# Optimization experiments

Measured on AMD Instinct MI355X. Metric: run time of the kernel, lower is better.

The kernel has to match this reference:

```python
import jax, jax.numpy as jnp
import numpy as np

B, C, H, W = 8, 128, 64, 64


def setup_inputs() -> dict:
    key = jax.random.key(0)
    ks = jax.random.split(key, 8)
    s = 1.0 / np.sqrt(C)
    return {
        "x1": jax.random.normal(ks[0], (B, C, H, W), dtype=jnp.float32),
        "x2": jax.random.normal(ks[1], (B, C, H, W), dtype=jnp.float32),
        "Wq": jax.random.normal(ks[2], (C, C), dtype=jnp.float32) * s,
        "bq": jax.random.normal(ks[3], (C,), dtype=jnp.float32) * s,
        "Wk": jax.random.normal(ks[4], (C, C), dtype=jnp.float32) * s,
        "bk": jax.random.normal(ks[5], (C,), dtype=jnp.float32) * s,
        "Wv": jax.random.normal(ks[6], (C, C), dtype=jnp.float32) * s,
        "bv": jax.random.normal(ks[7], (C,), dtype=jnp.float32) * s,
    }


def reference(x1, x2, Wq, bq, Wk, bk, Wv, bv):
    b, c, h, w = x1.shape
    n = h * w
    # 1x1 conv == channel matmul per pixel; flatten spatial dims -> [b, c, n]
    x1f = x1.reshape(b, c, n)
    x2f = x2.reshape(b, c, n)
    q = jnp.einsum("oc,bcn->bno", Wq, x1f) + bq[None, None, :]  # [b, n, c]
    k = jnp.einsum("oc,bcn->bon", Wk, x2f) + bk[None, :, None]  # [b, c, n]
    v = jnp.einsum("oc,bcn->bon", Wv, x2f) + bv[None, :, None]  # [b, c, n]
    energy = jnp.einsum("bnc,bcm->bnm", q, k)                   # [b, n, n] (unscaled)
    attention = jax.nn.softmax(energy, axis=-1)
    # out[b,c,i] = sum_j v[b,c,j] * attention[b,i,j]
    out = jnp.einsum("bcj,bij->bci", v, attention)
    return out.reshape(b, c, h, w)
```

## Files before the change

kernel.cpp:

```cpp
#include <hip/hip_runtime.h>

typedef float f4 __attribute__((ext_vector_type(4)));
typedef float f16v __attribute__((ext_vector_type(16)));
typedef _Float16 hf;
typedef __fp16 fp16x2 __attribute__((ext_vector_type(2)));
typedef hf h8 __attribute__((ext_vector_type(8)));
typedef unsigned short ushort_t;
typedef unsigned int uint_t;
typedef uint_t u4 __attribute__((ext_vector_type(4)));

#define BATCH 8
#define CH 128
#define NPIX 4096
#define LOG2E 1.4426950408889634f
#define RESCALE_THR 8.0f

__device__ inline f16v mfma32h(h8 a, h8 b, f16v c) {
    return __builtin_amdgcn_mfma_f32_32x32x16_f16(a, b, c, 0, 0, 0);
}

__device__ inline uint_t pk2h(float a, float b) {
    fp16x2 pp = __builtin_amdgcn_cvt_pkrtz(a, b);
    union { fp16x2 v; uint_t u; } cv;
    cv.v = pp;
    return cv.u;
}

__device__ inline void pl32swap(uint_t& a, uint_t& b) {
    asm("v_permlane32_swap_b32 %0, %1" : "+v"(a), "+v"(b));
}

typedef __attribute__((address_space(3))) uint_t lds_uint;
typedef __attribute__((address_space(1))) const uint_t global_uint;
__device__ inline void dma16(const void* g, void* l) {
    __builtin_amdgcn_global_load_lds((global_uint*)g, (lds_uint*)l, 16, 0, 0);
}

__device__ inline ushort_t h2u(hf x) {
    union { hf h; ushort_t u; } cv;
    cv.h = x;
    return cv.u;
}

__global__ __launch_bounds__(256) void qkv_kernel(const float* __restrict__ x1,
                                                  const float* __restrict__ x2,
                                                  const float* __restrict__ Wq,
                                                  const float* __restrict__ Wk,
                                                  const float* __restrict__ Wv,
                                                  const float* __restrict__ bq,
                                                  const float* __restrict__ bk,
                                                  const float* __restrict__ bv,
                                                  hf* __restrict__ Qf, hf* __restrict__ Kf,
                                                  hf* __restrict__ Vf) {
    __shared__ __align__(16) ushort_t XH[64 * 128];
    __shared__ __align__(16) ushort_t XL[64 * 128];

    int bid = blockIdx.x;
    int m = bid >> 9;
    int rem = bid & 511;
    int b = rem & 7;
    int n0 = (rem >> 3) << 6;

    const float* X = ((m == 0) ? x1 : x2) + (size_t)b * CH * NPIX;
    const float* bias = (m == 0) ? bq : (m == 1) ? bk : bv;

    int tid = threadIdx.x;
#pragma unroll
    for (int r = 0; r < 8; ++r) {
        int c = 16 * r + (tid >> 4);
        int n4 = (tid & 15) << 2;
        f4 v = *(const f4*)&X[(size_t)c * NPIX + n0 + n4];
        int cs = c >> 3, cj = c & 7;
#pragma unroll
        for (int j = 0; j < 4; ++j) {
            int n = n4 + j;
            hf hi = (hf)v[j];
            hf lo = (hf)(v[j] - (float)hi);
            int ofs = n * 128 + ((cs ^ (n & 15)) << 3) + cj;
            XH[ofs] = h2u(hi);
            XL[ofs] = h2u(lo);
        }
    }

    int lane = tid & 63;
    int w = tid >> 6;
    int h = lane >> 5;
    int m32 = lane & 31;
    int o0 = w * 32;

    const float* Wsrc = (m == 0) ? Wq : (m == 1) ? Wk : Wv;
    float wscale = (m == 0) ? LOG2E : 1.0f;
    h8 wf[8];
    {
        const float* wrow = Wsrc + (size_t)(o0 + m32) * CH;
#pragma unroll
        for (int kc = 0; kc < 8; ++kc) {
            f4 a = *(const f4*)&wrow[kc * 16 + h * 8];
            f4 b2 = *(const f4*)&wrow[kc * 16 + h * 8 + 4];
            h8 t;
#pragma unroll
            for (int j = 0; j < 4; ++j) {
                t[j] = (hf)(a[j] * wscale);
                t[4 + j] = (hf)(b2[j] * wscale);
            }
            wf[kc] = t;
        }
    }

    __syncthreads();

    f16v acc[2];
#pragma unroll
    for (int g = 0; g < 2; ++g)
#pragma unroll
        for (int r = 0; r < 16; ++r) acc[g][r] = 0.f;

    int swzn = m32 & 15;
#pragma unroll
    for (int g = 0; g < 2; ++g) {
        int nrow = (g * 32 + m32) * 128;
#pragma unroll
        for (int kc = 0; kc < 8; ++kc) {
            int sofs = nrow + (((kc * 2 + h) ^ swzn) << 3);
            h8 xh = *(const h8*)&XH[sofs];
            h8 xl = *(const h8*)&XL[sofs];
            if (m == 2) {
                acc[g] = mfma32h(wf[kc], xh, acc[g]);
                acc[g] = mfma32h(wf[kc], xl, acc[g]);
            } else {
                acc[g] = mfma32h(xh, wf[kc], acc[g]);
                acc[g] = mfma32h(xl, wf[kc], acc[g]);
            }
        }
    }

    if (m < 2) {
        float bval = bias[o0 + m32] * ((m == 0) ? LOG2E : 1.0f);
        hf* Y = ((m == 0) ? Qf : Kf) + (size_t)b * NPIX * CH;
#pragma unroll
        for (int g = 0; g < 2; ++g)
#pragma unroll
            for (int r = 0; r < 16; ++r) {
                int n = n0 + g * 32 + (r & 3) + 8 * (r >> 2) + 4 * h;
                Y[(size_t)n * CH + o0 + m32] = (hf)(acc[g][r] + bval);
            }
    } else {
        hf* Yv = Vf + (size_t)b * CH * NPIX;
#pragma unroll
        for (int g = 0; g < 2; ++g)
#pragma unroll
            for (int r = 0; r < 16; ++r) {
                int o = o0 + (r & 3) + 8 * (r >> 2) + 4 * h;
                Yv[(size_t)o * NPIX + n0 + g * 32 + m32] = (hf)(acc[g][r] + bias[o]);
            }
    }
}

__global__ __launch_bounds__(256, 3) void attn_kernel(const hf* __restrict__ Qf,
                                                      const hf* __restrict__ Kf,
                                                      const hf* __restrict__ Vf,
                                                      hf* __restrict__ Opart,
                                                      float* __restrict__ Mpart,
                                                      float* __restrict__ Lpart) {
    __shared__ __align__(16) ushort_t smem[24576];

    int tid = threadIdx.x;
    int lane = tid & 63;
    int w = tid >> 6;
    int h = lane >> 5;
    int m32 = lane & 31;

    int idx = blockIdx.x;
    int b = idx & 7;
    int ks = (idx >> 3) & 3;
    int qt = idx >> 5;
    int q0 = (qt << 7) + w * 32;
    int k0g = ks << 10;

    const hf* Qb = Qf + (size_t)b * NPIX * CH;
    const hf* Kb = Kf + (size_t)b * NPIX * CH;
    const hf* Vb = Vf + (size_t)b * CH * NPIX;

    h8 qf[8];
#pragma unroll
    for (int kc = 0; kc < 8; ++kc)
        qf[kc] = *(const h8*)&Qb[(size_t)(q0 + m32) * CH + kc * 16 + h * 8];

    const hf* pK[2];
    const hf* pV[2];
#pragma unroll
    for (int a = 0; a < 2; ++a) {
        int chunk_hi = w * 2 + a;
        int rowk = chunk_hi * 4 + (lane >> 4);
        int lck = (lane & 15) ^ (rowk & 15);
        pK[a] = Kb + (size_t)(k0g + rowk) * CH + lck * 8;
        int rowv = chunk_hi * 16 + (lane >> 2);
        int lcv = (lane & 3) ^ (rowv & 3) ^ ((rowv >> 2) & 1);
        pV[a] = Vb + (size_t)rowv * NPIX + k0g + lcv * 8;
    }

#pragma unroll
    for (int tp = 0; tp < 2; ++tp) {
#pragma unroll
        for (int a = 0; a < 2; ++a) {
            dma16(pK[a], &smem[tp * 4096 + (w * 2 + a) * 512]);
            dma16(pV[a], &smem[12288 + tp * 4096 + (w * 2 + a) * 512]);
            pK[a] += 32 * CH;
            pV[a] += 32;
        }
    }

    f16v accO[4];
#pragma unroll
    for (int ct = 0; ct < 4; ++ct)
#pragma unroll
        for (int r = 0; r < 16; ++r) accO[ct][r] = 0.f;
    float mprev = -1e30f;
    float lsum = 0.f;

    int pvs[2];
#pragma unroll
    for (int g2 = 0; g2 < 2; ++g2)
        pvs[g2] = (g2 * 2 + h) ^ (m32 & 3) ^ ((m32 >> 2) & 1);

    int br = 0, bw = 2;
    for (int t = 0; t < 32; ++t) {
        if (t < 31) asm volatile("s_waitcnt vmcnt(4) lgkmcnt(0)" ::: "memory");
        else        asm volatile("s_waitcnt vmcnt(0) lgkmcnt(0)" ::: "memory");
        __builtin_amdgcn_s_barrier();
        __builtin_amdgcn_sched_barrier(0);

        if (t < 30) {
#pragma unroll
            for (int a = 0; a < 2; ++a) {
                dma16(pK[a], &smem[bw * 4096 + (w * 2 + a) * 512]);
                dma16(pV[a], &smem[12288 + bw * 4096 + (w * 2 + a) * 512]);
                pK[a] += 32 * CH;
                pV[a] += 32;
            }
        }
        const ushort_t* kb = smem + br * 4096;
        const ushort_t* vb = smem + 12288 + br * 4096;

        f16v acc;
#pragma unroll
        for (int r = 0; r < 16; ++r) acc[r] = 0.f;
        __builtin_amdgcn_s_setprio(1);
#pragma unroll
        for (int kc = 0; kc < 8; ++kc) {
            int pA = (kc * 2 + h) ^ (m32 & 15);
            h8 ahi = *(const h8*)&kb[m32 * 128 + pA * 8];
            acc = mfma32h(ahi, qf[kc], acc);
        }
        __builtin_amdgcn_s_setprio(0);

        float ta = fmaxf(fmaxf(acc[0], acc[1]), acc[2]);
        float tb = fmaxf(fmaxf(acc[3], acc[4]), acc[5]);
        ta = fmaxf(fmaxf(ta, acc[6]), acc[7]);
        tb = fmaxf(fmaxf(tb, acc[8]), acc[9]);
        ta = fmaxf(fmaxf(ta, acc[10]), acc[11]);
        tb = fmaxf(fmaxf(tb, acc[12]), acc[13]);
        ta = fmaxf(fmaxf(ta, acc[14]), acc[15]);
        float tmax = fmaxf(ta, tb);
        if (__any(tmax > mprev + RESCALE_THR)) {
            float tx = fmaxf(tmax, __shfl_xor(tmax, 32));
            float mnew = fmaxf(mprev, tx);
            float alpha = exp2f(mprev - mnew);
            lsum *= alpha;
#pragma unroll
            for (int ct = 0; ct < 4; ++ct)
#pragma unroll
                for (int r = 0; r < 16; ++r) accO[ct][r] *= alpha;
            mprev = mnew;
        }

        uint_t pk[8];
        float ps0 = 0.f, ps1 = 0.f;
#pragma unroll
        for (int t2 = 0; t2 < 8; ++t2) {
            float e0 = exp2f(acc[2 * t2] - mprev);
            float e1 = exp2f(acc[2 * t2 + 1] - mprev);
            ps0 += e0;
            ps1 += e1;
            pk[t2] = pk2h(e0, e1);
        }
        lsum += ps0 + ps1;

        pl32swap(pk[0], pk[2]);
        pl32swap(pk[1], pk[3]);
        pl32swap(pk[4], pk[6]);
        pl32swap(pk[5], pk[7]);
        h8 pbp[2];
#pragma unroll
        for (int g2 = 0; g2 < 2; ++g2) {
            u4 fv;
            fv[0] = pk[g2 * 4 + 0];
            fv[1] = pk[g2 * 4 + 1];
            fv[2] = pk[g2 * 4 + 2];
            fv[3] = pk[g2 * 4 + 3];
            __builtin_memcpy(&pbp[g2], &fv, 16);
        }

        __builtin_amdgcn_s_setprio(1);
#pragma unroll
        for (int g2 = 0; g2 < 2; ++g2) {
            int pv = pvs[g2];
#pragma unroll
            for (int ct = 0; ct < 4; ++ct) {
                h8 av = *(const h8*)&vb[(ct * 32 + m32) * 32 + pv * 8];
                accO[ct] = mfma32h(av, pbp[g2], accO[ct]);
            }
        }
        __builtin_amdgcn_s_setprio(0);

        br = (br == 2) ? 0 : br + 1;
        bw = (bw == 2) ? 0 : bw + 1;
    }

    lsum += __shfl_xor(lsum, 32);

    size_t base = (((size_t)ks * 8 + b) * 32 + qt) * 16384;
    size_t mlb = (((size_t)ks * 8 + b) * 32 + qt) * 128;
    int q = w * 32 + m32;
#pragma unroll
    for (int ct = 0; ct < 4; ++ct)
#pragma unroll
        for (int r = 0; r < 16; ++r) {
            int ch = ct * 32 + (r & 3) + 8 * (r >> 2) + 4 * h;
            Opart[base + ch * 128 + q] = (hf)accO[ct][r];
        }
    if (h == 0) {
        Mpart[mlb + q] = mprev;
        Lpart[mlb + q] = lsum;
    }
}

__global__ __launch_bounds__(256) void combine_kernel(const hf* __restrict__ Opart,
                                                      const float* __restrict__ Mp,
                                                      const float* __restrict__ Lp,
                                                      float* __restrict__ out) {
    int idx = blockIdx.x;
    int chh = idx & 1;
    int b = (idx >> 1) & 7;
    int qt = idx >> 4;
    int tid = threadIdx.x;
    int q8 = (tid & 15) << 3;
    int chl = tid >> 4;

    size_t tile = (size_t)b * 32 + qt;

    float Marr[4][8], Larr[4][8];
#pragma unroll
    for (int p = 0; p < 4; ++p) {
        const float* mp_ = Mp + ((size_t)p * 256 + tile) * 128 + q8;
        const float* lp_ = Lp + ((size_t)p * 256 + tile) * 128 + q8;
        f4 ma = *(const f4*)mp_;
        f4 mb = *(const f4*)(mp_ + 4);
        f4 la = *(const f4*)lp_;
        f4 lb = *(const f4*)(lp_ + 4);
#pragma unroll
        for (int j = 0; j < 4; ++j) {
            Marr[p][j] = ma[j];
            Marr[p][4 + j] = mb[j];
            Larr[p][j] = la[j];
            Larr[p][4 + j] = lb[j];
        }
    }

    float wgt[4][8];
#pragma unroll
    for (int j = 0; j < 8; ++j) {
        float M = fmaxf(fmaxf(Marr[0][j], Marr[1][j]), fmaxf(Marr[2][j], Marr[3][j]));
        float L = 0.f;
#pragma unroll
        for (int p = 0; p < 4; ++p) {
            float w_ = exp2f(Marr[p][j] - M);
            wgt[p][j] = w_;
            L += w_ * Larr[p][j];
        }
        float rd = 1.0f / L;
#pragma unroll
        for (int p = 0; p < 4; ++p) wgt[p][j] *= rd;
    }

    const hf* ob[4];
#pragma unroll
    for (int p = 0; p < 4; ++p) ob[p] = Opart + ((size_t)p * 256 + tile) * 16384 + q8;
    float* O = out + (size_t)b * CH * NPIX + (size_t)qt * 128 + q8;

#pragma unroll
    for (int it = 0; it < 4; ++it) {
        int ch = chh * 64 + it * 16 + chl;
        union { u4 u; h8 v; } o4[4];
#pragma unroll
        for (int p = 0; p < 4; ++p) o4[p].u = *(const u4*)&ob[p][(size_t)ch * 128];
        f4 r0, r1;
#pragma unroll
        for (int j = 0; j < 8; ++j) {
            float s = 0.f;
#pragma unroll
            for (int p = 0; p < 4; ++p) s += wgt[p][j] * (float)o4[p].v[j];
            if (j < 4) r0[j] = s;
            else r1[j - 4] = s;
        }
        float* dst = O + (size_t)ch * NPIX;
        *(f4*)dst = r0;
        *(f4*)(dst + 4) = r1;
    }
}

extern "C" void kernel_launch(void* const* d_in, const int* in_sizes, int n_in,
                              void* d_out, int out_size, void* d_ws, size_t ws_size,
                              hipStream_t stream) {
    const float* x1 = (const float*)d_in[0];
    const float* x2 = (const float*)d_in[1];
    const float* Wq = (const float*)d_in[2];
    const float* bq = (const float*)d_in[3];
    const float* Wk = (const float*)d_in[4];
    const float* bk = (const float*)d_in[5];
    const float* Wv = (const float*)d_in[6];
    const float* bv = (const float*)d_in[7];
    float* outp = (float*)d_out;

    const size_t N = (size_t)BATCH * NPIX * CH;
    hf* Qf = (hf*)d_ws;
    hf* Kf = Qf + N;
    hf* Vf = Qf + 2 * N;
    hf* Opart = Qf + 3 * N;
    float* Mp = (float*)(Opart + (size_t)4 * 8 * 32 * 16384);
    float* Lp = Mp + (size_t)4 * 8 * 32 * 128;

    qkv_kernel<<<3 * BATCH * (NPIX / 64), 256, 0, stream>>>(x1, x2, Wq, Wk, Wv,
                                                            bq, bk, bv, Qf, Kf, Vf);
    attn_kernel<<<BATCH * 4 * (NPIX / 128), 256, 0, stream>>>(Qf, Kf, Vf, Opart, Mp, Lp);
    combine_kernel<<<2 * BATCH * (NPIX / 128), 256, 0, stream>>>(Opart, Mp, Lp, outp);
}
```

Measured before the change: 209.9 us.

## Halve key splits and deepen attention LDS pipeline to four buffers

The attention kernel now splits the key range into 2 parts instead of 4, so each block walks 2048 keys. The combine kernel merges 2 partials instead of 4, which cuts partial-output traffic. The K/V staging ring grows from 3 to 4 LDS buffers with an explicitly unrolled schedule that keeps three tiles in flight, and occupancy drops from 3 to 2 blocks per CU because LDS use rises. The grid halves to 512 blocks, which may underfill the GPU's CUs and leave more of the latency exposed.

```diff
diff --git a/kernel.cpp b/kernel.cpp
--- a/kernel.cpp
+++ b/kernel.cpp
@@ -41,6 +41,13 @@
     cv.h = x;
     return cv.u;
 }
+
+#define WAITB(vm)                                                          \
+    do {                                                                   \
+        asm volatile("s_waitcnt vmcnt(" #vm ") lgkmcnt(0)" ::: "memory");  \
+        __builtin_amdgcn_s_barrier();                                      \
+        __builtin_amdgcn_sched_barrier(0);                                 \
+    } while (0)
 
 __global__ __launch_bounds__(256) void qkv_kernel(const float* __restrict__ x1,
                                                   const float* __restrict__ x2,
@@ -156,13 +163,13 @@
     }
 }
 
-__global__ __launch_bounds__(256, 3) void attn_kernel(const hf* __restrict__ Qf,
+__global__ __launch_bounds__(256, 2) void attn_kernel(const hf* __restrict__ Qf,
                                                       const hf* __restrict__ Kf,
                                                       const hf* __restrict__ Vf,
                                                       hf* __restrict__ Opart,
                                                       float* __restrict__ Mpart,
                                                       float* __restrict__ Lpart) {
-    __shared__ __align__(16) ushort_t smem[24576];
+    __shared__ __align__(16) ushort_t smem[32768];
 
     int tid = threadIdx.x;
     int lane = tid & 63;
@@ -172,10 +179,10 @@
 
     int idx = blockIdx.x;
     int b = idx & 7;
-    int ks = (idx >> 3) & 3;
-    int qt = idx >> 5;
+    int ks = (idx >> 3) & 1;
+    int qt = idx >> 4;
     int q0 = (qt << 7) + w * 32;
-    int k0g = ks << 10;
+    int k0g = ks << 11;
 
     const hf* Qb = Qf + (size_t)b * NPIX * CH;
     const hf* Kb = Kf + (size_t)b * NPIX * CH;
@@ -199,17 +206,6 @@
         pV[a] = Vb + (size_t)rowv * NPIX + k0g + lcv * 8;
     }
 
-#pragma unroll
-    for (int tp = 0; tp < 2; ++tp) {
-#pragma unroll
-        for (int a = 0; a < 2; ++a) {
-            dma16(pK[a], &smem[tp * 4096 + (w * 2 + a) * 512]);
-            dma16(pV[a], &smem[12288 + tp * 4096 + (w * 2 + a) * 512]);
-            pK[a] += 32 * CH;
-            pV[a] += 32;
-        }
-    }
-
     f16v accO[4];
 #pragma unroll
     for (int ct = 0; ct < 4; ++ct)
@@ -223,24 +219,19 @@
     for (int g2 = 0; g2 < 2; ++g2)
         pvs[g2] = (g2 * 2 + h) ^ (m32 & 3) ^ ((m32 >> 2) & 1);
 
-    int br = 0, bw = 2;
-    for (int t = 0; t < 32; ++t) {
-        if (t < 31) asm volatile("s_waitcnt vmcnt(4) lgkmcnt(0)" ::: "memory");
-        else        asm volatile("s_waitcnt vmcnt(0) lgkmcnt(0)" ::: "memory");
-        __builtin_amdgcn_s_barrier();
-        __builtin_amdgcn_sched_barrier(0);
-
-        if (t < 30) {
-#pragma unroll
-            for (int a = 0; a < 2; ++a) {
-                dma16(pK[a], &smem[bw * 4096 + (w * 2 + a) * 512]);
-                dma16(pV[a], &smem[12288 + bw * 4096 + (w * 2 + a) * 512]);
-                pK[a] += 32 * CH;
-                pV[a] += 32;
-            }
-        }
-        const ushort_t* kb = smem + br * 4096;
-        const ushort_t* vb = smem + 12288 + br * 4096;
+    auto stage = [&](int bufw) {
+#pragma unroll
+        for (int a = 0; a < 2; ++a) {
+            dma16(pK[a], &smem[bufw * 4096 + (w * 2 + a) * 512]);
+            dma16(pV[a], &smem[16384 + bufw * 4096 + (w * 2 + a) * 512]);
+            pK[a] += 32 * CH;
+            pV[a] += 32;
+        }
+    };
+
+    auto comp = [&](int bufr) {
+        const ushort_t* kb = smem + bufr * 4096;
+        const ushort_t* vb = smem + 16384 + bufr * 4096;
 
         f16v acc;
 #pragma unroll
@@ -312,10 +303,22 @@
             }
         }
         __builtin_amdgcn_s_setprio(0);
-
-        br = (br == 2) ? 0 : br + 1;
-        bw = (bw == 2) ? 0 : bw + 1;
-    }
+    };
+
+    stage(0);
+    stage(1);
+    stage(2);
+
+    for (int tb = 0; tb < 15; ++tb) {
+        WAITB(8); stage(3); comp(0);
+        WAITB(8); stage(0); comp(1);
+        WAITB(8); stage(1); comp(2);
+        WAITB(8); stage(2); comp(3);
+    }
+    WAITB(8); stage(3); comp(0);
+    WAITB(8); comp(1);
+    WAITB(4); comp(2);
+    WAITB(0); comp(3);
 
     lsum += __shfl_xor(lsum, 32);
 
@@ -349,9 +352,9 @@
 
     size_t tile = (size_t)b * 32 + qt;
 
-    float Marr[4][8], Larr[4][8];
-#pragma unroll
-    for (int p = 0; p < 4; ++p) {
+    float Marr[2][8], Larr[2][8];
+#pragma unroll
+    for (int p = 0; p < 2; ++p) {
         const float* mp_ = Mp + ((size_t)p * 256 + tile) * 128 + q8;
         const float* lp_ = Lp + ((size_t)p * 256 + tile) * 128 + q8;
         f4 ma = *(const f4*)mp_;
@@ -367,39 +370,32 @@
         }
     }
 
-    float wgt[4][8];
+    float wgt[2][8];
 #pragma unroll
     for (int j = 0; j < 8; ++j) {
-        float M = fmaxf(fmaxf(Marr[0][j], Marr[1][j]), fmaxf(Marr[2][j], Marr[3][j]));
-        float L = 0.f;
-#pragma unroll
-        for (int p = 0; p < 4; ++p) {
-            float w_ = exp2f(Marr[p][j] - M);
-            wgt[p][j] = w_;
-            L += w_ * Larr[p][j];
-        }
-        float rd = 1.0f / L;
-#pragma unroll
-        for (int p = 0; p < 4; ++p) wgt[p][j] *= rd;
-    }
-
-    const hf* ob[4];
-#pragma unroll
-    for (int p = 0; p < 4; ++p) ob[p] = Opart + ((size_t)p * 256 + tile) * 16384 + q8;
+        float M = fmaxf(Marr[0][j], Marr[1][j]);
+        float w0 = exp2f(Marr[0][j] - M);
+        float w1 = exp2f(Marr[1][j] - M);
+        float rd = 1.0f / (w0 * Larr[0][j] + w1 * Larr[1][j]);
+        wgt[0][j] = w0 * rd;
+        wgt[1][j] = w1 * rd;
+    }
+
+    const hf* ob[2];
+#pragma unroll
+    for (int p = 0; p < 2; ++p) ob[p] = Opart + ((size_t)p * 256 + tile) * 16384 + q8;
     float* O = out + (size_t)b * CH * NPIX + (size_t)qt * 128 + q8;
 
 #pragma unroll
     for (int it = 0; it < 4; ++it) {
         int ch = chh * 64 + it * 16 + chl;
-        union { u4 u; h8 v; } o4[4];
-#pragma unroll
-        for (int p = 0; p < 4; ++p) o4[p].u = *(const u4*)&ob[p][(size_t)ch * 128];
+        union { u4 u; h8 v; } o4[2];
+#pragma unroll
+        for (int p = 0; p < 2; ++p) o4[p].u = *(const u4*)&ob[p][(size_t)ch * 128];
         f4 r0, r1;
 #pragma unroll
         for (int j = 0; j < 8; ++j) {
-            float s = 0.f;
-#pragma unroll
-            for (int p = 0; p < 4; ++p) s += wgt[p][j] * (float)o4[p].v[j];
+            float s = wgt[0][j] * (float)o4[0].v[j] + wgt[1][j] * (float)o4[1].v[j];
             if (j < 4) r0[j] = s;
             else r1[j - 4] = s;
         }
@@ -427,11 +423,11 @@
     hf* Kf = Qf + N;
     hf* Vf = Qf + 2 * N;
     hf* Opart = Qf + 3 * N;
-    float* Mp = (float*)(Opart + (size_t)4 * 8 * 32 * 16384);
-    float* Lp = Mp + (size_t)4 * 8 * 32 * 128;
+    float* Mp = (float*)(Opart + (size_t)2 * 8 * 32 * 16384);
+    float* Lp = Mp + (size_t)2 * 8 * 32 * 128;
 
     qkv_kernel<<<3 * BATCH * (NPIX / 64), 256, 0, stream>>>(x1, x2, Wq, Wk, Wv,
                                                             bq, bk, bv, Qf, Kf, Vf);
-    attn_kernel<<<BATCH * 4 * (NPIX / 128), 256, 0, stream>>>(Qf, Kf, Vf, Opart, Mp, Lp);
+    attn_kernel<<<BATCH * 2 * (NPIX / 128), 256, 0, stream>>>(Qf, Kf, Vf, Opart, Mp, Lp);
     combine_kernel<<<2 * BATCH * (NPIX / 128), 256, 0, stream>>>(Opart, Mp, Lp, outp);
 }
```

Result: faster. 201.0 us, median of 2 (-4.3%).

## Split attention block into 64-query tiles with channel-split waves and Q in LDS

Applied to the files above, without the earlier changes.

Each attention block now handles 64 queries instead of 128. Its four waves split as 2 query groups by 2 channel halves, so each wave holds two output accumulators instead of four, and occupancy rises to 4 blocks per CU. Q is staged into LDS once and read per MFMA instead of held in registers. The K/V pipeline moves from triple to double buffering with an extra barrier per step. The grid doubles and the combine kernel is adjusted to the new partial layout. In exchange, QK^T work is duplicated across the channel-split waves, and the extra LDS reads and barriers add cost.

```diff
diff --git a/kernel.cpp b/kernel.cpp
--- a/kernel.cpp
+++ b/kernel.cpp
@@ -41,6 +41,19 @@
     cv.h = x;
     return cv.u;
 }
+
+#define WAITB(vm)                                                          \
+    do {                                                                   \
+        asm volatile("s_waitcnt vmcnt(" #vm ") lgkmcnt(0)" ::: "memory");  \
+        __builtin_amdgcn_s_barrier();                                      \
+        __builtin_amdgcn_sched_barrier(0);                                 \
+    } while (0)
+
+#define BARB()                              \
+    do {                                    \
+        __builtin_amdgcn_s_barrier();       \
+        __builtin_amdgcn_sched_barrier(0);  \
+    } while (0)
 
 __global__ __launch_bounds__(256) void qkv_kernel(const float* __restrict__ x1,
                                                   const float* __restrict__ x2,
@@ -156,7 +169,7 @@
     }
 }
 
-__global__ __launch_bounds__(256, 3) void attn_kernel(const hf* __restrict__ Qf,
+__global__ __launch_bounds__(256, 4) void attn_kernel(const hf* __restrict__ Qf,
                                                       const hf* __restrict__ Kf,
                                                       const hf* __restrict__ Vf,
                                                       hf* __restrict__ Opart,
@@ -169,78 +182,72 @@
     int w = tid >> 6;
     int h = lane >> 5;
     int m32 = lane & 31;
+    int qg = w >> 1;
+    int cg = w & 1;
 
     int idx = blockIdx.x;
     int b = idx & 7;
     int ks = (idx >> 3) & 3;
     int qt = idx >> 5;
-    int q0 = (qt << 7) + w * 32;
     int k0g = ks << 10;
 
     const hf* Qb = Qf + (size_t)b * NPIX * CH;
     const hf* Kb = Kf + (size_t)b * NPIX * CH;
     const hf* Vb = Vf + (size_t)b * CH * NPIX;
 
-    h8 qf[8];
-#pragma unroll
-    for (int kc = 0; kc < 8; ++kc)
-        qf[kc] = *(const h8*)&Qb[(size_t)(q0 + m32) * CH + kc * 16 + h * 8];
+    {
+        const hf* pQ[4];
+#pragma unroll
+        for (int a = 0; a < 4; ++a) {
+            int cq = w * 4 + a;
+            int rowq = cq * 4 + (lane >> 4);
+            int lcq = (lane & 15) ^ (rowq & 15);
+            pQ[a] = Qb + (size_t)((qt << 6) + rowq) * CH + lcq * 8;
+        }
+#pragma unroll
+        for (int a = 0; a < 4; ++a) dma16(pQ[a], &smem[(w * 4 + a) * 512]);
+    }
 
     const hf* pK[2];
     const hf* pV[2];
 #pragma unroll
     for (int a = 0; a < 2; ++a) {
-        int chunk_hi = w * 2 + a;
-        int rowk = chunk_hi * 4 + (lane >> 4);
+        int c8 = w * 2 + a;
+        int rowk = c8 * 4 + (lane >> 4);
         int lck = (lane & 15) ^ (rowk & 15);
         pK[a] = Kb + (size_t)(k0g + rowk) * CH + lck * 8;
-        int rowv = chunk_hi * 16 + (lane >> 2);
+        int rowv = c8 * 16 + (lane >> 2);
         int lcv = (lane & 3) ^ (rowv & 3) ^ ((rowv >> 2) & 1);
         pV[a] = Vb + (size_t)rowv * NPIX + k0g + lcv * 8;
     }
 
-#pragma unroll
-    for (int tp = 0; tp < 2; ++tp) {
+    auto stage = [&](int buf) {
 #pragma unroll
         for (int a = 0; a < 2; ++a) {
-            dma16(pK[a], &smem[tp * 4096 + (w * 2 + a) * 512]);
-            dma16(pV[a], &smem[12288 + tp * 4096 + (w * 2 + a) * 512]);
+            int c8 = w * 2 + a;
+            dma16(pK[a], &smem[8192 + buf * 4096 + c8 * 512]);
+            dma16(pV[a], &smem[16384 + buf * 4096 + c8 * 512]);
             pK[a] += 32 * CH;
             pV[a] += 32;
         }
-    }
-
-    f16v accO[4];
-#pragma unroll
-    for (int ct = 0; ct < 4; ++ct)
-#pragma unroll
-        for (int r = 0; r < 16; ++r) accO[ct][r] = 0.f;
+    };
+
+    stage(0);
+
+    f16v accO[2];
+#pragma unroll
+    for (int j = 0; j < 2; ++j)
+#pragma unroll
+        for (int r = 0; r < 16; ++r) accO[j][r] = 0.f;
     float mprev = -1e30f;
     float lsum = 0.f;
 
-    int pvs[2];
-#pragma unroll
-    for (int g2 = 0; g2 < 2; ++g2)
-        pvs[g2] = (g2 * 2 + h) ^ (m32 & 3) ^ ((m32 >> 2) & 1);
-
-    int br = 0, bw = 2;
-    for (int t = 0; t < 32; ++t) {
-        if (t < 31) asm volatile("s_waitcnt vmcnt(4) lgkmcnt(0)" ::: "memory");
-        else        asm volatile("s_waitcnt vmcnt(0) lgkmcnt(0)" ::: "memory");
-        __builtin_amdgcn_s_barrier();
-        __builtin_amdgcn_sched_barrier(0);
-
-        if (t < 30) {
-#pragma unroll
-            for (int a = 0; a < 2; ++a) {
-                dma16(pK[a], &smem[bw * 4096 + (w * 2 + a) * 512]);
-                dma16(pV[a], &smem[12288 + bw * 4096 + (w * 2 + a) * 512]);
-                pK[a] += 32 * CH;
-                pV[a] += 32;
-            }
-        }
-        const ushort_t* kb = smem + br * 4096;
-        const ushort_t* vb = smem + 12288 + br * 4096;
+    int rq128 = (qg * 32 + m32) * 128;
+    int sw15 = m32 & 15;
+
+    auto comp = [&](int buf) {
+        const ushort_t* kb = smem + 8192 + buf * 4096;
+        const ushort_t* vb = smem + 16384 + buf * 4096;
 
         f16v acc;
 #pragma unroll
@@ -248,9 +255,10 @@
         __builtin_amdgcn_s_setprio(1);
 #pragma unroll
         for (int kc = 0; kc < 8; ++kc) {
-            int pA = (kc * 2 + h) ^ (m32 & 15);
+            int pA = (kc * 2 + h) ^ sw15;
             h8 ahi = *(const h8*)&kb[m32 * 128 + pA * 8];
-            acc = mfma32h(ahi, qf[kc], acc);
+            h8 qv = *(const h8*)&smem[rq128 + pA * 8];
+            acc = mfma32h(ahi, qv, acc);
         }
         __builtin_amdgcn_s_setprio(0);
 
@@ -268,9 +276,9 @@
             float alpha = exp2f(mprev - mnew);
             lsum *= alpha;
 #pragma unroll
-            for (int ct = 0; ct < 4; ++ct)
-#pragma unroll
-                for (int r = 0; r < 16; ++r) accO[ct][r] *= alpha;
+            for (int j = 0; j < 2; ++j)
+#pragma unroll
+                for (int r = 0; r < 16; ++r) accO[j][r] *= alpha;
             mprev = mnew;
         }
 
@@ -304,32 +312,37 @@
         __builtin_amdgcn_s_setprio(1);
 #pragma unroll
         for (int g2 = 0; g2 < 2; ++g2) {
-            int pv = pvs[g2];
-#pragma unroll
-            for (int ct = 0; ct < 4; ++ct) {
+            int pv = (g2 * 2 + h) ^ (m32 & 3) ^ ((m32 >> 2) & 1);
+#pragma unroll
+            for (int j = 0; j < 2; ++j) {
+                int ct = cg * 2 + j;
                 h8 av = *(const h8*)&vb[(ct * 32 + m32) * 32 + pv * 8];
-                accO[ct] = mfma32h(av, pbp[g2], accO[ct]);
+                accO[j] = mfma32h(av, pbp[g2], accO[j]);
             }
         }
         __builtin_amdgcn_s_setprio(0);
-
-        br = (br == 2) ? 0 : br + 1;
-        bw = (bw == 2) ? 0 : bw + 1;
-    }
+    };
+
+    for (int tb = 0; tb < 15; ++tb) {
+        stage(1); WAITB(4); comp(0); BARB();
+        stage(0); WAITB(4); comp(1); BARB();
+    }
+    stage(1); WAITB(4); comp(0); BARB();
+    WAITB(0); comp(1);
 
     lsum += __shfl_xor(lsum, 32);
 
-    size_t base = (((size_t)ks * 8 + b) * 32 + qt) * 16384;
-    size_t mlb = (((size_t)ks * 8 + b) * 32 + qt) * 128;
-    int q = w * 32 + m32;
-#pragma unroll
-    for (int ct = 0; ct < 4; ++ct)
+    size_t base = (((size_t)ks * 8 + b) * 64 + qt) * 8192;
+    size_t mlb = (((size_t)ks * 8 + b) * 64 + qt) * 64;
+    int q = qg * 32 + m32;
+#pragma unroll
+    for (int j = 0; j < 2; ++j)
 #pragma unroll
         for (int r = 0; r < 16; ++r) {
-            int ch = ct * 32 + (r & 3) + 8 * (r >> 2) + 4 * h;
-            Opart[base + ch * 128 + q] = (hf)accO[ct][r];
-        }
-    if (h == 0) {
+            int ch = (cg * 2 + j) * 32 + (r & 3) + 8 * (r >> 2) + 4 * h;
+            Opart[base + ch * 64 + q] = (hf)accO[j][r];
+        }
+    if (cg == 0 && h == 0) {
         Mpart[mlb + q] = mprev;
         Lpart[mlb + q] = lsum;
     }
@@ -344,24 +357,21 @@
     int b = (idx >> 1) & 7;
     int qt = idx >> 4;
     int tid = threadIdx.x;
-    int q8 = (tid & 15) << 3;
-    int chl = tid >> 4;
-
-    size_t tile = (size_t)b * 32 + qt;
+    int q8 = (tid & 7) << 3;
+    int chl = tid >> 3;
 
     float Marr[4][8], Larr[4][8];
 #pragma unroll
     for (int p = 0; p < 4; ++p) {
-        const float* mp_ = Mp + ((size_t)p * 256 + tile) * 128 + q8;
-        const float* lp_ = Lp + ((size_t)p * 256 + tile) * 128 + q8;
-        f4 ma = *(const f4*)mp_;
-        f4 mb = *(const f4*)(mp_ + 4);
-        f4 la = *(const f4*)lp_;
-        f4 lb = *(const f4*)(lp_ + 4);
+        size_t mb = (((size_t)p * 8 + b) * 64 + qt) * 64 + q8;
+        f4 ma = *(const f4*)&Mp[mb];
+        f4 mb2 = *(const f4*)&Mp[mb + 4];
+        f4 la = *(const f4*)&Lp[mb];
+        f4 lb = *(const f4*)&Lp[mb + 4];
 #pragma unroll
         for (int j = 0; j < 4; ++j) {
             Marr[p][j] = ma[j];
-            Marr[p][4 + j] = mb[j];
+            Marr[p][4 + j] = mb2[j];
             Larr[p][j] = la[j];
             Larr[p][4 + j] = lb[j];
         }
@@ -385,15 +395,16 @@
 
     const hf* ob[4];
 #pragma unroll
-    for (int p = 0; p < 4; ++p) ob[p] = Opart + ((size_t)p * 256 + tile) * 16384 + q8;
-    float* O = out + (size_t)b * CH * NPIX + (size_t)qt * 128 + q8;
-
-#pragma unroll
-    for (int it = 0; it < 4; ++it) {
-        int ch = chh * 64 + it * 16 + chl;
+    for (int p = 0; p < 4; ++p)
+        ob[p] = Opart + (((size_t)p * 8 + b) * 64 + qt) * 8192 + q8;
+    float* O = out + (size_t)b * CH * NPIX + (qt << 6) + q8;
+
+#pragma unroll
+    for (int it = 0; it < 2; ++it) {
+        int ch = chh * 64 + it * 32 + chl;
         union { u4 u; h8 v; } o4[4];
 #pragma unroll
-        for (int p = 0; p < 4; ++p) o4[p].u = *(const u4*)&ob[p][(size_t)ch * 128];
+        for (int p = 0; p < 4; ++p) o4[p].u = *(const u4*)&ob[p][(size_t)ch * 64];
         f4 r0, r1;
 #pragma unroll
         for (int j = 0; j < 8; ++j) {
@@ -427,11 +438,11 @@
     hf* Kf = Qf + N;
     hf* Vf = Qf + 2 * N;
     hf* Opart = Qf + 3 * N;
-    float* Mp = (float*)(Opart + (size_t)4 * 8 * 32 * 16384);
-    float* Lp = Mp + (size_t)4 * 8 * 32 * 128;
+    float* Mp = (float*)(Opart + (size_t)4 * 8 * 64 * 8192);
+    float* Lp = Mp + (size_t)4 * 8 * 64 * 64;
 
     qkv_kernel<<<3 * BATCH * (NPIX / 64), 256, 0, stream>>>(x1, x2, Wq, Wk, Wv,
                                                             bq, bk, bv, Qf, Kf, Vf);
-    attn_kernel<<<BATCH * 4 * (NPIX / 128), 256, 0, stream>>>(Qf, Kf, Vf, Opart, Mp, Lp);
-    combine_kernel<<<2 * BATCH * (NPIX / 128), 256, 0, stream>>>(Opart, Mp, Lp, outp);
-}
+    attn_kernel<<<BATCH * 4 * (NPIX / 64), 256, 0, stream>>>(Qf, Kf, Vf, Opart, Mp, Lp);
+    combine_kernel<<<2 * BATCH * (NPIX / 64), 256, 0, stream>>>(Opart, Mp, Lp, outp);
+}
```

Result: slower. 278.2 us (+32.5%).
